# Performance work log

Measured on AMD Instinct MI355X. Metric: run time of the kernel, lower is better.

The kernel has to match this reference:

```python
import jax, jax.numpy as jnp
import numpy as np

B, D, H, L = 131072, 128, 128, 4
LN_EPS = 1e-5


def _layernorm(x, gamma, beta):
    mu = jnp.mean(x, axis=-1, keepdims=True)
    var = jnp.mean(jnp.square(x - mu), axis=-1, keepdims=True)
    return (x - mu) * jax.lax.rsqrt(var + LN_EPS) * gamma + beta


def setup_inputs() -> dict:
    key = jax.random.key(0)
    ks = jax.random.split(key, 12)
    t = jax.random.uniform(ks[0], (1,), dtype=jnp.float32)
    p = jax.random.normal(ks[1], (B, D), dtype=jnp.float32)
    w = jax.random.normal(ks[2], (B, D), dtype=jnp.float32)
    # VectorField parameters (torch default inits approximated with scaled normals)
    W_in = jax.random.normal(ks[3], (H, D), dtype=jnp.float32) * (1.0 / np.sqrt(D))
    b_in = jax.random.normal(ks[4], (H,), dtype=jnp.float32) * 0.01
    # FourierFeature buffers, scale=1.0 (hard-coded in VectorField)
    fw = jax.random.normal(ks[5], (L, H), dtype=jnp.float32) * 1.0
    fb = jax.random.uniform(ks[6], (L, H), dtype=jnp.float32) * 1.0
    gamma = jnp.ones((L, H), dtype=jnp.float32)
    beta = jnp.zeros((L, H), dtype=jnp.float32)
    Wl = jax.random.normal(ks[7], (L, H, H), dtype=jnp.float32) * (1.0 / np.sqrt(H))
    bl = jax.random.normal(ks[8], (L, H), dtype=jnp.float32) * 0.01
    W_out = jax.random.normal(ks[9], (D, H), dtype=jnp.float32) * (1.0 / np.sqrt(H))
    b_out = jax.random.normal(ks[10], (D,), dtype=jnp.float32) * 0.01
    return {"t": t, "p": p, "w": w, "W_in": W_in, "b_in": b_in, "fw": fw,
            "fb": fb, "gamma": gamma, "beta": beta, "Wl": Wl, "bl": bl,
            "W_out": W_out, "b_out": b_out}


def reference(t, p, w, W_in, b_in, fw, fb, gamma, beta, Wl, bl, W_out, b_out):
    # VectorField.forward: all ops act per-row, so batched vjp == vmapped per-sample vjp
    def vf(pp):  # pp: [B, D]
        h = pp @ W_in.T + b_in                      # [B, H]
        for i in range(L):
            h = h + jnp.sin(t * fw[i] + fb[i])      # time embedding, broadcast [H]
            h = jax.nn.softplus(h)
            h = _layernorm(h, gamma[i], beta[i])
            h = h @ Wl[i].T + bl[i]
        return h @ W_out.T + b_out                  # [B, D]

    dp, vjp_fn = jax.vjp(vf, p)
    dw = -vjp_fn(w)[0]
    return dp, dw
```

## Files before the change

### kernel.cpp

```cpp
#include <hip/hip_runtime.h>

typedef unsigned short u16;
typedef unsigned int   u32;
typedef __attribute__((ext_vector_type(8))) short bf16x8;
typedef __attribute__((ext_vector_type(4))) float f32x4;
typedef __attribute__((ext_vector_type(2))) unsigned int u32x2;

#define NB 131072
#define LN_EPS 1e-5f
#define EX_STRIDE 136

__device__ __forceinline__ u16 f2b(float f){
  union { __bf16 h; u16 u; } c; c.h = (__bf16)f; return c.u;
}
__device__ __forceinline__ u32 pk2(float a, float b){
  return (u32)f2b(a) | ((u32)f2b(b) << 16);
}
__device__ __forceinline__ float upk(u32 pr, int hi){
  union { u32 u; float f; } c; c.u = hi ? (pr & 0xFFFF0000u) : (pr << 16); return c.f;
}
__device__ __forceinline__ float qsum(float x){
  x += __shfl_xor(x, 16);
  x += __shfl_xor(x, 32);
  return x;
}
__device__ __forceinline__ bf16x8 cvt8(const float* __restrict__ s){
  f32x4 x0 = *(const f32x4*)s;
  f32x4 x1 = *(const f32x4*)(s + 4);
  bf16x8 r;
  r[0]=(short)f2b(x0[0]); r[1]=(short)f2b(x0[1]);
  r[2]=(short)f2b(x0[2]); r[3]=(short)f2b(x0[3]);
  r[4]=(short)f2b(x1[0]); r[5]=(short)f2b(x1[1]);
  r[6]=(short)f2b(x1[2]); r[7]=(short)f2b(x1[3]);
  return r;
}

__device__ __forceinline__ void glds16(const u16* g, u16* l){
  __builtin_amdgcn_global_load_lds(
      (const __attribute__((address_space(1))) void*)g,
      (__attribute__((address_space(3))) void*)l, 16, 0, 0);
}
__device__ __forceinline__ void stageB(const u16* __restrict__ packB, int m,
                                       u16* __restrict__ bst, int wave, int lane){
  const u16* src = packB + m*16384 + wave*512 + lane*8;
  u16*       dst = bst   + wave*512;
  #pragma unroll
  for (int k = 0; k < 8; k++)
    glds16(src + k*2048, dst + k*2048);
}

__device__ __forceinline__ void gemm16s(const bf16x8 x[4], const u16* __restrict__ Blds,
                                        int lane, f32x4 C[8]){
  const bf16x8* Wf = (const bf16x8*)Blds;
  #pragma unroll
  for (int mt = 0; mt < 8; mt++){
    f32x4 c = {0.f, 0.f, 0.f, 0.f};
    #pragma unroll
    for (int kt = 0; kt < 4; kt++){
      bf16x8 wfrag = Wf[(mt*4 + kt)*64 + lane];
      c = __builtin_amdgcn_mfma_f32_16x16x32_bf16(wfrag, x[kt], c, 0, 0, 0);
    }
    C[mt] = c;
  }
}

__global__ void prep_kernel(const float* __restrict__ t,   const float* __restrict__ W_in,
                            const float* __restrict__ b_in,const float* __restrict__ fw,
                            const float* __restrict__ fb,  const float* __restrict__ gamma,
                            const float* __restrict__ beta,const float* __restrict__ Wl,
                            const float* __restrict__ bl,  const float* __restrict__ W_out,
                            const float* __restrict__ b_out,
                            u16* __restrict__ packB, float* __restrict__ vecs)
{
  int bid = blockIdx.x, tid = threadIdx.x;
  if (bid < 768){
    int e    = bid*256 + tid;
    int m    = e >> 14;
    int r    = e & 16383;
    int fi   = r >> 9;
    int lane = (r >> 3) & 63;
    int j    = r & 7;
    int nt = fi >> 2, kt = fi & 3;
    int k = kt*32 + (lane >> 4)*8 + j;
    int n = nt*16 + (lane & 15);
    const float* src; bool tr;
    if      (m == 0){ src = W_in;              tr = true;  }
    else if (m <= 4){ src = Wl + (m-1)*16384;  tr = true;  }
    else if (m == 5){ src = W_out;             tr = true;  }
    else if (m == 6){ src = W_out;             tr = false; }
    else if (m <=10){ src = Wl + (m-7)*16384;  tr = false; }
    else            { src = W_in;              tr = false; }
    float v = tr ? src[n*128 + k] : src[k*128 + n];
    if      (m >= 1 && m <= 4)  v *= gamma[(m-1)*128 + k];
    else if (m >= 7 && m <= 10) v *= gamma[(m-7)*128 + n];
    packB[e] = f2b(v);
  } else if (bid < 770){
    int idx = (bid - 768)*256 + tid;
    vecs[idx] = sinf(t[0] * fw[idx] + fb[idx]);
  } else if (bid < 772){
    int gid = (bid - 770)*256 + tid;
    int i = gid >> 7, o = gid & 127;
    const float* Wr = Wl + i*16384 + o*128;
    const float* be = beta + i*128;
    float acc = bl[gid];
    for (int k2 = 0; k2 < 128; k2++) acc += be[k2] * Wr[k2];
    vecs[512 + gid] = acc;
  } else {
    if (tid < 128) vecs[1024 + tid]        = b_in[tid];
    else           vecs[1152 + (tid-128)]  = b_out[tid-128];
  }
}

__global__ __launch_bounds__(256, 2)
void fused_vf(const float* __restrict__ p, const float* __restrict__ w,
              const u16* __restrict__ packB, const float* __restrict__ vecs,
              float* __restrict__ dp_out, float* __restrict__ dw_out)
{
  __shared__ __align__(16) u16  exch[4 * 16 * EX_STRIDE];
  __shared__ __align__(16) u16  bstage[16384];
  __shared__ __align__(16) float sv[1024];

  const int tid  = threadIdx.x;
  const int wave = tid >> 6, lane = tid & 63;
  const int l15  = lane & 15, quad = lane >> 4;
  u16* ex = exch + wave * 16 * EX_STRIDE;
  u16*       exw = ex + l15*EX_STRIDE + quad*4;
  const u16* exr = ex + l15*EX_STRIDE + quad*8;

  stageB(packB, 0, bstage, wave, lane);
  for (int idx = tid; idx < 1024; idx += 256) sv[idx] = vecs[idx];
  const float* sS    = sv;
  const float* sBl   = sv + 512;
  const float* gBin  = vecs + 1024;
  const float* gBout = vecs + 1152;

  const long rowBase = (long)blockIdx.x * 64 + wave * 16;

  u32   sp_ck[4][8][2];
  float mus[4];
  float invs[4];

  bf16x8 x[4];
  f32x4  C[8];

  {
    const float* pr = p + (size_t)(rowBase + l15)*128 + quad*8;
    #pragma unroll
    for (int kt = 0; kt < 4; kt++) x[kt] = cvt8(pr + kt*32);
  }
  __syncthreads();
  gemm16s(x, bstage, lane, C);
  #pragma unroll
  for (int mt = 0; mt < 8; mt++)
    C[mt] += *(const f32x4*)(gBin + mt*16 + quad*4);

  #pragma unroll
  for (int i = 0; i < 4; i++){
    __syncthreads();
    stageB(packB, 1+i, bstage, wave, lane);
    float sum = 0.f, ssq = 0.f;
    #pragma unroll
    for (int mt = 0; mt < 8; mt++){
      f32x4 se = *(const f32x4*)(sS + i*128 + mt*16 + quad*4);
      #pragma unroll
      for (int r = 0; r < 4; r++){
        float a_ = C[mt][r] + se[r];
        float e  = __expf(-fabsf(a_));
        float sp = fmaxf(a_, 0.0f) + __logf(1.0f + e);
        u16 sb = f2b(sp);
        if (r & 1) sp_ck[i][mt][r>>1] |= ((u32)sb) << 16; else sp_ck[i][mt][r>>1] = sb;
        sum += sp; ssq += sp*sp;
        C[mt][r] = sp;
      }
    }
    float m1 = qsum(sum) * (1.0f/128.0f);
    float m2 = qsum(ssq) * (1.0f/128.0f);
    float inv = rsqrtf(fmaxf(m2 - m1*m1, 0.0f) + LN_EPS);
    mus[i] = m1; invs[i] = inv;
    #pragma unroll
    for (int mt = 0; mt < 8; mt++){
      u32x2 v;
      v[0] = pk2((C[mt][0]-m1)*inv, (C[mt][1]-m1)*inv);
      v[1] = pk2((C[mt][2]-m1)*inv, (C[mt][3]-m1)*inv);
      *(u32x2*)(exw + mt*16) = v;
    }
    __syncthreads();
    #pragma unroll
    for (int kt = 0; kt < 4; kt++) x[kt] = *(const bf16x8*)(exr + kt*32);
    gemm16s(x, bstage, lane, C);
    #pragma unroll
    for (int mt = 0; mt < 8; mt++)
      C[mt] += *(const f32x4*)(sBl + i*128 + mt*16 + quad*4);
  }

  __syncthreads();
  stageB(packB, 5, bstage, wave, lane);
  #pragma unroll
  for (int mt = 0; mt < 8; mt++){
    u32x2 v;
    v[0] = pk2(C[mt][0], C[mt][1]);
    v[1] = pk2(C[mt][2], C[mt][3]);
    *(u32x2*)(exw + mt*16) = v;
  }
  __syncthreads();
  #pragma unroll
  for (int kt = 0; kt < 4; kt++) x[kt] = *(const bf16x8*)(exr + kt*32);
  gemm16s(x, bstage, lane, C);
  {
    float* gp = dp_out + (size_t)(rowBase + l15)*128;
    #pragma unroll
    for (int mt = 0; mt < 8; mt++){
      f32x4 o = C[mt] + *(const f32x4*)(gBout + mt*16 + quad*4);
      *(f32x4*)(gp + mt*16 + quad*4) = o;
    }
  }

  __syncthreads();
  stageB(packB, 6, bstage, wave, lane);
  {
    const float* wr = w + (size_t)(rowBase + l15)*128 + quad*8;
    #pragma unroll
    for (int kt = 0; kt < 4; kt++) x[kt] = cvt8(wr + kt*32);
  }
  __syncthreads();
  gemm16s(x, bstage, lane, C);
  __syncthreads();
  stageB(packB, 10, bstage, wave, lane);

  #pragma unroll
  for (int ii = 0; ii < 4; ii++){
    const int i = 3 - ii;
    #pragma unroll
    for (int mt = 0; mt < 8; mt++){
      u32x2 v;
      v[0] = pk2(C[mt][0], C[mt][1]);
      v[1] = pk2(C[mt][2], C[mt][3]);
      *(u32x2*)(exw + mt*16) = v;
    }
    __syncthreads();
    #pragma unroll
    for (int kt = 0; kt < 4; kt++) x[kt] = *(const bf16x8*)(exr + kt*32);
    gemm16s(x, bstage, lane, C);
    __syncthreads();
    stageB(packB, (ii < 3) ? (7 + (2 - ii)) : 11, bstage, wave, lane);
    float s1 = 0.f, s2 = 0.f;
    #pragma unroll
    for (int mt = 0; mt < 8; mt++)
      #pragma unroll
      for (int r = 0; r < 4; r++){
        float sp = upk(sp_ck[i][mt][r>>1], r & 1);
        float xh = (sp - mus[i]) * invs[i];
        float gx = C[mt][r];
        s1 += gx; s2 += gx * xh;
      }
    float m1 = qsum(s1) * (1.0f/128.0f);
    float m2 = qsum(s2) * (1.0f/128.0f);
    #pragma unroll
    for (int mt = 0; mt < 8; mt++)
      #pragma unroll
      for (int r = 0; r < 4; r++){
        float sp = upk(sp_ck[i][mt][r>>1], r & 1);
        float xh = (sp - mus[i]) * invs[i];
        float sg = 1.0f - __expf(-sp);
        float gu = invs[i] * (C[mt][r] - m1 - xh * m2);
        C[mt][r] = gu * sg;
      }
  }

  #pragma unroll
  for (int mt = 0; mt < 8; mt++){
    u32x2 v;
    v[0] = pk2(C[mt][0], C[mt][1]);
    v[1] = pk2(C[mt][2], C[mt][3]);
    *(u32x2*)(exw + mt*16) = v;
  }
  __syncthreads();
  #pragma unroll
  for (int kt = 0; kt < 4; kt++) x[kt] = *(const bf16x8*)(exr + kt*32);
  gemm16s(x, bstage, lane, C);
  {
    float* gp = dw_out + (size_t)(rowBase + l15)*128;
    #pragma unroll
    for (int mt = 0; mt < 8; mt++){
      f32x4 o = -C[mt];
      *(f32x4*)(gp + mt*16 + quad*4) = o;
    }
  }
}

extern "C" void kernel_launch(void* const* d_in, const int* in_sizes, int n_in,
                              void* d_out, int out_size, void* d_ws, size_t ws_size,
                              hipStream_t stream)
{
  const float* t     = (const float*)d_in[0];
  const float* p     = (const float*)d_in[1];
  const float* w     = (const float*)d_in[2];
  const float* W_in  = (const float*)d_in[3];
  const float* b_in  = (const float*)d_in[4];
  const float* fw    = (const float*)d_in[5];
  const float* fb    = (const float*)d_in[6];
  const float* gamma = (const float*)d_in[7];
  const float* beta  = (const float*)d_in[8];
  const float* Wl    = (const float*)d_in[9];
  const float* bl    = (const float*)d_in[10];
  const float* W_out = (const float*)d_in[11];
  const float* b_out = (const float*)d_in[12];

  u16*   packB = (u16*)d_ws;
  float* vecs  = (float*)((char*)d_ws + 12*16384*2);

  prep_kernel<<<773, 256, 0, stream>>>(t, W_in, b_in, fw, fb, gamma, beta,
                                       Wl, bl, W_out, b_out, packB, vecs);

  float* dp = (float*)d_out;
  float* dw = (float*)d_out + (size_t)NB * 128;
  fused_vf<<<NB/64, 256, 0, stream>>>(p, w, packB, vecs, dp, dw);
}
```

Baseline: 356.3 us.

## Replace LDS exchange with cross-lane shuffles and fold time embedding into biases

The accumulator-to-operand layout transpose between chained MFMA GEMMs now uses ds_bpermute-style __shfl calls instead of writing to and reading back from a shared-memory exchange buffer. This drops the exchange LDS allocation, which may raise occupancy. The prep kernel also folds the sin time embedding into the preceding bias vectors, removing a per-layer add and its LDS load. The cost is 32 shuffles plus selects per transpose, and some remaining __syncthreads around the exchange are kept even though they now only guard the staged weights.

```diff
diff --git a/kernel.cpp b/kernel.cpp
--- a/kernel.cpp
+++ b/kernel.cpp
@@ -4,11 +4,9 @@
 typedef unsigned int   u32;
 typedef __attribute__((ext_vector_type(8))) short bf16x8;
 typedef __attribute__((ext_vector_type(4))) float f32x4;
-typedef __attribute__((ext_vector_type(2))) unsigned int u32x2;
 
 #define NB 131072
 #define LN_EPS 1e-5f
-#define EX_STRIDE 136
 
 __device__ __forceinline__ u16 f2b(float f){
   union { __bf16 h; u16 u; } c; c.h = (__bf16)f; return c.u;
@@ -61,6 +59,27 @@
       c = __builtin_amdgcn_mfma_f32_16x16x32_bf16(wfrag, x[kt], c, 0, 0, 0);
     }
     C[mt] = c;
+  }
+}
+
+__device__ __forceinline__ void pulls(const u32 pk[8][2], int sl0, int sl1,
+                                      bool odd, bf16x8 x[4]){
+  #pragma unroll
+  for (int kt = 0; kt < 4; kt++){
+    union { u32 u[4]; bf16x8 v; } r;
+    u32 e0 = (u32)__shfl((int)pk[2*kt  ][0], sl0, 64);
+    u32 e1 = (u32)__shfl((int)pk[2*kt  ][1], sl0, 64);
+    u32 e2 = (u32)__shfl((int)pk[2*kt  ][0], sl1, 64);
+    u32 e3 = (u32)__shfl((int)pk[2*kt  ][1], sl1, 64);
+    u32 o0 = (u32)__shfl((int)pk[2*kt+1][0], sl0, 64);
+    u32 o1 = (u32)__shfl((int)pk[2*kt+1][1], sl0, 64);
+    u32 o2 = (u32)__shfl((int)pk[2*kt+1][0], sl1, 64);
+    u32 o3 = (u32)__shfl((int)pk[2*kt+1][1], sl1, 64);
+    r.u[0] = odd ? o0 : e0;
+    r.u[1] = odd ? o1 : e1;
+    r.u[2] = odd ? o2 : e2;
+    r.u[3] = odd ? o3 : e3;
+    x[kt] = r.v;
   }
 }
 
@@ -94,20 +113,29 @@
     if      (m >= 1 && m <= 4)  v *= gamma[(m-1)*128 + k];
     else if (m >= 7 && m <= 10) v *= gamma[(m-7)*128 + n];
     packB[e] = f2b(v);
-  } else if (bid < 770){
-    int idx = (bid - 768)*256 + tid;
-    vecs[idx] = sinf(t[0] * fw[idx] + fb[idx]);
-  } else if (bid < 772){
-    int gid = (bid - 770)*256 + tid;
-    int i = gid >> 7, o = gid & 127;
-    const float* Wr = Wl + i*16384 + o*128;
-    const float* be = beta + i*128;
-    float acc = bl[gid];
-    for (int k2 = 0; k2 < 128; k2++) acc += be[k2] * Wr[k2];
-    vecs[512 + gid] = acc;
   } else {
-    if (tid < 128) vecs[1024 + tid]        = b_in[tid];
-    else           vecs[1152 + (tid-128)]  = b_out[tid-128];
+    int gid = (bid - 768)*256 + tid;
+    int vec = gid >> 7, o = gid & 127;
+    float v;
+    if (vec == 0){
+      v = b_in[o] + sinf(t[0]*fw[o] + fb[o]);
+    } else if (vec <= 3){
+      int i = vec - 1;
+      const float* Wr = Wl + i*16384 + o*128;
+      const float* be = beta + i*128;
+      float acc = bl[i*128 + o];
+      for (int k2 = 0; k2 < 128; k2++) acc += be[k2]*Wr[k2];
+      v = acc + sinf(t[0]*fw[vec*128 + o] + fb[vec*128 + o]);
+    } else if (vec == 4){
+      const float* Wr = Wl + 3*16384 + o*128;
+      const float* be = beta + 3*128;
+      float acc = bl[3*128 + o];
+      for (int k2 = 0; k2 < 128; k2++) acc += be[k2]*Wr[k2];
+      v = acc;
+    } else {
+      v = b_out[o];
+    }
+    vecs[gid] = v;
   }
 }
 
@@ -116,23 +144,20 @@
               const u16* __restrict__ packB, const float* __restrict__ vecs,
               float* __restrict__ dp_out, float* __restrict__ dw_out)
 {
-  __shared__ __align__(16) u16  exch[4 * 16 * EX_STRIDE];
   __shared__ __align__(16) u16  bstage[16384];
-  __shared__ __align__(16) float sv[1024];
+  __shared__ __align__(16) float sv[768];
 
   const int tid  = threadIdx.x;
   const int wave = tid >> 6, lane = tid & 63;
   const int l15  = lane & 15, quad = lane >> 4;
-  u16* ex = exch + wave * 16 * EX_STRIDE;
-  u16*       exw = ex + l15*EX_STRIDE + quad*4;
-  const u16* exr = ex + l15*EX_STRIDE + quad*8;
+  const int sl0  = ((quad & 1) << 5) + l15;
+  const int sl1  = sl0 + 16;
+  const bool odd = (quad >> 1) != 0;
 
   stageB(packB, 0, bstage, wave, lane);
-  for (int idx = tid; idx < 1024; idx += 256) sv[idx] = vecs[idx];
-  const float* sS    = sv;
-  const float* sBl   = sv + 512;
-  const float* gBin  = vecs + 1024;
-  const float* gBout = vecs + 1152;
+  for (int idx = tid; idx < 768; idx += 256) sv[idx] = vecs[idx];
+  const float* sCb   = sv;
+  const float* sBout = sv + 640;
 
   const long rowBase = (long)blockIdx.x * 64 + wave * 16;
 
@@ -152,7 +177,7 @@
   gemm16s(x, bstage, lane, C);
   #pragma unroll
   for (int mt = 0; mt < 8; mt++)
-    C[mt] += *(const f32x4*)(gBin + mt*16 + quad*4);
+    C[mt] += *(const f32x4*)(sCb + mt*16 + quad*4);
 
   #pragma unroll
   for (int i = 0; i < 4; i++){
@@ -161,10 +186,9 @@
     float sum = 0.f, ssq = 0.f;
     #pragma unroll
     for (int mt = 0; mt < 8; mt++){
-      f32x4 se = *(const f32x4*)(sS + i*128 + mt*16 + quad*4);
       #pragma unroll
       for (int r = 0; r < 4; r++){
-        float a_ = C[mt][r] + se[r];
+        float a_ = C[mt][r];
         float e  = __expf(-fabsf(a_));
         float sp = fmaxf(a_, 0.0f) + __logf(1.0f + e);
         u16 sb = f2b(sp);
@@ -177,40 +201,40 @@
     float m2 = qsum(ssq) * (1.0f/128.0f);
     float inv = rsqrtf(fmaxf(m2 - m1*m1, 0.0f) + LN_EPS);
     mus[i] = m1; invs[i] = inv;
-    #pragma unroll
-    for (int mt = 0; mt < 8; mt++){
-      u32x2 v;
-      v[0] = pk2((C[mt][0]-m1)*inv, (C[mt][1]-m1)*inv);
-      v[1] = pk2((C[mt][2]-m1)*inv, (C[mt][3]-m1)*inv);
-      *(u32x2*)(exw + mt*16) = v;
+    {
+      u32 pk[8][2];
+      #pragma unroll
+      for (int mt = 0; mt < 8; mt++){
+        pk[mt][0] = pk2((C[mt][0]-m1)*inv, (C[mt][1]-m1)*inv);
+        pk[mt][1] = pk2((C[mt][2]-m1)*inv, (C[mt][3]-m1)*inv);
+      }
+      pulls(pk, sl0, sl1, odd, x);
     }
     __syncthreads();
-    #pragma unroll
-    for (int kt = 0; kt < 4; kt++) x[kt] = *(const bf16x8*)(exr + kt*32);
     gemm16s(x, bstage, lane, C);
     #pragma unroll
     for (int mt = 0; mt < 8; mt++)
-      C[mt] += *(const f32x4*)(sBl + i*128 + mt*16 + quad*4);
+      C[mt] += *(const f32x4*)(sCb + (i+1)*128 + mt*16 + quad*4);
   }
 
   __syncthreads();
   stageB(packB, 5, bstage, wave, lane);
-  #pragma unroll
-  for (int mt = 0; mt < 8; mt++){
-    u32x2 v;
-    v[0] = pk2(C[mt][0], C[mt][1]);
-    v[1] = pk2(C[mt][2], C[mt][3]);
-    *(u32x2*)(exw + mt*16) = v;
-  }
-  __syncthreads();
-  #pragma unroll
-  for (int kt = 0; kt < 4; kt++) x[kt] = *(const bf16x8*)(exr + kt*32);
+  {
+    u32 pk[8][2];
+    #pragma unroll
+    for (int mt = 0; mt < 8; mt++){
+      pk[mt][0] = pk2(C[mt][0], C[mt][1]);
+      pk[mt][1] = pk2(C[mt][2], C[mt][3]);
+    }
+    pulls(pk, sl0, sl1, odd, x);
+  }
+  __syncthreads();
   gemm16s(x, bstage, lane, C);
   {
     float* gp = dp_out + (size_t)(rowBase + l15)*128;
     #pragma unroll
     for (int mt = 0; mt < 8; mt++){
-      f32x4 o = C[mt] + *(const f32x4*)(gBout + mt*16 + quad*4);
+      f32x4 o = C[mt] + *(const f32x4*)(sBout + mt*16 + quad*4);
       *(f32x4*)(gp + mt*16 + quad*4) = o;
     }
   }
@@ -230,16 +254,16 @@
   #pragma unroll
   for (int ii = 0; ii < 4; ii++){
     const int i = 3 - ii;
-    #pragma unroll
-    for (int mt = 0; mt < 8; mt++){
-      u32x2 v;
-      v[0] = pk2(C[mt][0], C[mt][1]);
-      v[1] = pk2(C[mt][2], C[mt][3]);
-      *(u32x2*)(exw + mt*16) = v;
+    {
+      u32 pk[8][2];
+      #pragma unroll
+      for (int mt = 0; mt < 8; mt++){
+        pk[mt][0] = pk2(C[mt][0], C[mt][1]);
+        pk[mt][1] = pk2(C[mt][2], C[mt][3]);
+      }
+      pulls(pk, sl0, sl1, odd, x);
     }
     __syncthreads();
-    #pragma unroll
-    for (int kt = 0; kt < 4; kt++) x[kt] = *(const bf16x8*)(exr + kt*32);
     gemm16s(x, bstage, lane, C);
     __syncthreads();
     stageB(packB, (ii < 3) ? (7 + (2 - ii)) : 11, bstage, wave, lane);
@@ -267,16 +291,16 @@
       }
   }
 
-  #pragma unroll
-  for (int mt = 0; mt < 8; mt++){
-    u32x2 v;
-    v[0] = pk2(C[mt][0], C[mt][1]);
-    v[1] = pk2(C[mt][2], C[mt][3]);
-    *(u32x2*)(exw + mt*16) = v;
-  }
-  __syncthreads();
-  #pragma unroll
-  for (int kt = 0; kt < 4; kt++) x[kt] = *(const bf16x8*)(exr + kt*32);
+  {
+    u32 pk[8][2];
+    #pragma unroll
+    for (int mt = 0; mt < 8; mt++){
+      pk[mt][0] = pk2(C[mt][0], C[mt][1]);
+      pk[mt][1] = pk2(C[mt][2], C[mt][3]);
+    }
+    pulls(pk, sl0, sl1, odd, x);
+  }
+  __syncthreads();
   gemm16s(x, bstage, lane, C);
   {
     float* gp = dw_out + (size_t)(rowBase + l15)*128;
@@ -309,7 +333,7 @@
   u16*   packB = (u16*)d_ws;
   float* vecs  = (float*)((char*)d_ws + 12*16384*2);
 
-  prep_kernel<<<773, 256, 0, stream>>>(t, W_in, b_in, fw, fb, gamma, beta,
+  prep_kernel<<<771, 256, 0, stream>>>(t, W_in, b_in, fw, fb, gamma, beta,
                                        Wl, bl, W_out, b_out, packB, vecs);
 
   float* dp = (float*)d_out;
```

Result: slower. 385.8 us (+8.3%).
